# Kernel optimization log

Measured on AMD Instinct MI355X. Metric: run time of the kernel, lower is better.

## Reference

```python
import jax, jax.numpy as jnp
import numpy as np

L_MAX = 3
NUM_SHELLS = 4
GAUSS_SCALE = 16.0

def monomial_basis_3D(d):
    monoms = []
    for I in range((d + 1) ** 3):
        i = I % (d + 1)
        a = (I - i) // (d + 1)
        j = a % (d + 1)
        k = (a - j) // (d + 1)
        if i + j + k <= d:
            monoms.append((i, j, k))
    return sorted(set(monoms))

_MONOMS = np.array(monomial_basis_3D(L_MAX), dtype=np.float32)  # [20, 3]
_SH_IDX = np.concatenate([np.full(2 * l + 1, l) for l in range(L_MAX + 1)]).astype(np.int32)  # [16]
_N_SH = _SH_IDX.shape[0]  # 16


def setup_inputs() -> dict:
    key = jax.random.key(0)
    k1, k2 = jax.random.split(key)
    # points roughly inside/near the unit ball so the bound mask is nontrivial
    patches = jax.random.normal(k1, (8, 2048, 32, 3), dtype=jnp.float32) * 0.35
    Y = jax.random.normal(k2, (_N_SH, _MONOMS.shape[0]), dtype=jnp.float32)
    return {"patches": patches, "Y": Y}


def reference(patches, Y):
    m_exp = jnp.asarray(_MONOMS)                      # [M, 3] float exponents
    sh_idx = jnp.asarray(_SH_IDX)                     # [n_sh]
    # one-hot map from sh channel -> degree l, for the per-degree l2 reduction
    deg_onehot = jax.nn.one_hot(sh_idx, L_MAX + 1, dtype=patches.dtype)  # [n_sh, L+1]

    dist = jnp.linalg.norm(patches, axis=-1, keepdims=True)              # [B,V,P,1]
    normed = -(patches / jnp.maximum(dist, 1e-6))                        # transpose=True

    # monomial basis: prod_c normed[...,c]^e_c  -> [B,V,P,M]
    monoms = jnp.prod(jnp.power(normed[..., None, :], m_exp), axis=-1)
    sh = jnp.einsum('ij,bvpj->bvpi', Y, monoms)                          # [B,V,P,n_sh]

    # gaussian radial shells
    rad = jnp.arange(NUM_SHELLS, dtype=patches.dtype) / (NUM_SHELLS - 1) # [S]
    shells = jnp.exp(-GAUSS_SCALE * (dist - rad) ** 2)                   # [B,V,P,S]
    shells = shells / jnp.maximum(jnp.sum(shells, axis=-1, keepdims=True), 1e-6)
    shells = shells[..., None, :]                                        # [B,V,P,1,S]
    shells = jnp.where(dist[..., None] <= 1.0, shells, 0.0)              # bound mask

    sh_patches = shells * sh[..., None]                                  # [B,V,P,n_sh,S]

    # per-degree L2 normalization over the patch axis
    l2 = jnp.sum(sh_patches * sh_patches, axis=2, keepdims=True)         # [B,V,1,n_sh,S]
    ml = jnp.sqrt(jnp.einsum('bvoms,ml->bvols', l2, deg_onehot))         # [B,V,1,L+1,S]
    ml = jnp.mean(ml, axis=1, keepdims=True)                             # [B,1,1,L+1,S]
    ml = jnp.maximum(ml, 1e-8)
    norm = jnp.take(ml, sh_idx, axis=-2)                                 # [B,1,1,n_sh,S]
    return sh_patches / norm
```

## Files before the change

kernel.cpp:

```cpp
#include <hip/hip_runtime.h>

typedef float f32x4 __attribute__((ext_vector_type(4)));


__device__ __forceinline__ void compute_monoms(float nx, float ny, float nz, float* m) {
    float zp2 = nz*nz, zp3 = zp2*nz;
    float yp2 = ny*ny, yp3 = yp2*ny;
    float xp2 = nx*nx, xp3 = xp2*nx;
    m[0]=1.0f;  m[1]=nz;       m[2]=zp2;      m[3]=zp3;
    m[4]=ny;    m[5]=ny*nz;    m[6]=ny*zp2;
    m[7]=yp2;   m[8]=yp2*nz;   m[9]=yp3;
    m[10]=nx;   m[11]=nx*nz;   m[12]=nx*zp2;
    m[13]=nx*ny; m[14]=nx*ny*nz; m[15]=nx*yp2;
    m[16]=xp2;  m[17]=xp2*nz;  m[18]=xp2*ny;
    m[19]=xp3;
}

__device__ __forceinline__ void compute_shells(float dist, float* sl) {
    const float B1 = 32.0f/3.0f, B2 = 64.0f/3.0f, B3 = 32.0f;
    const float C1 = -16.0f/9.0f, C2 = -64.0f/9.0f, C3 = -16.0f;
    float nd2 = -16.0f * dist * dist;
    sl[0] = __expf(nd2);
    sl[1] = __expf(fmaf(B1, dist, nd2 + C1));
    sl[2] = __expf(fmaf(B2, dist, nd2 + C2));
    sl[3] = __expf(fmaf(B3, dist, nd2 + C3));
    float den = sl[0] + sl[1] + sl[2] + sl[3];
    float r = 1.0f / fmaxf(den, 1e-6f);
    float mask = (dist <= 1.0f) ? r : 0.0f;
#pragma unroll
    for (int s = 0; s < 4; ++s) sl[s] *= mask;
}

__global__ __launch_bounds__(256) void sh_k1(const float* __restrict__ patches,
                                             const float* __restrict__ Y,
                                             float* __restrict__ partials) {
    __shared__ float sh2_lds[8][32][17];
    __shared__ float shl2_lds[8][32][5];
    __shared__ float l2_lds[8][16][4];
    __shared__ float red[8][16];

    const int tid  = threadIdx.x;
    const int wv   = tid >> 6;
    const int lane = tid & 63;
    const int half = lane >> 5;
    const int p    = lane & 31;
    const int u    = wv * 2 + half;
    const int unit = blockIdx.x * 8 + u;

    const float* pp = patches + ((size_t)unit * 32 + p) * 3;
    float x = pp[0], y = pp[1], z = pp[2];
    float dist = sqrtf(x*x + y*y + z*z);
    float inv  = 1.0f / fmaxf(dist, 1e-6f);
    float nx = -x*inv, ny = -y*inv, nz = -z*inv;
    float m[20];
    compute_monoms(nx, ny, nz, m);

#pragma unroll
    for (int i = 0; i < 16; ++i) {
        float acc = 0.f;
#pragma unroll
        for (int j = 0; j < 20; ++j)
            acc = fmaf(Y[i*20 + j], m[j], acc);
        sh2_lds[u][p][i] = acc * acc;
    }
    float sl[4];
    compute_shells(dist, sl);
#pragma unroll
    for (int s = 0; s < 4; ++s) shl2_lds[u][p][s] = sl[s]*sl[s];
    __syncthreads();

    const int ri = lane >> 2, rs = lane & 3;
    const int u0 = wv*2, u1 = wv*2 + 1;
    float acc0 = 0.f, acc1 = 0.f;
#pragma unroll
    for (int q = 0; q < 32; ++q) {
        acc0 = fmaf(sh2_lds[u0][q][ri], shl2_lds[u0][q][rs], acc0);
        acc1 = fmaf(sh2_lds[u1][q][ri], shl2_lds[u1][q][rs], acc1);
    }
    l2_lds[u0][ri][rs] = acc0;
    l2_lds[u1][ri][rs] = acc1;
    __syncthreads();

    if (lane < 32) {
        const int h2 = lane >> 4;
        const int c  = lane & 15;
        const int l  = c >> 2, s = c & 3;
        const int uu = wv*2 + h2;
        const int start = l*l, cnt = 2*l + 1;
        float acc = 0.f;
        for (int t = 0; t < cnt; ++t) acc += l2_lds[uu][start + t][s];
        red[uu][c] = sqrtf(acc);
    }
    __syncthreads();
    if (tid < 16) {
        float s2 = 0.f;
#pragma unroll
        for (int uu = 0; uu < 8; ++uu) s2 += red[uu][tid];
        partials[blockIdx.x*16 + tid] = s2;
    }
}

__global__ __launch_bounds__(256) void sh_k3(const float* __restrict__ patches,
                                             const float* __restrict__ Y,
                                             const float* __restrict__ partials,
                                             f32x4* __restrict__ out) {
    __shared__ float mon[256][12];
    __shared__ float pr[16][17];
    __shared__ float rcp_lds[16];

    const int tid = threadIdx.x;
    const int blk = blockIdx.x;
    const int bb  = blk >> 8;

    const int ch = tid & 15, r0 = tid >> 4;
    float pl[16];
#pragma unroll
    for (int r = 0; r < 16; ++r)
        pl[r] = partials[((size_t)bb*256 + r0 + r*16)*16 + ch];

    {
        const size_t ptg = (size_t)blk*256 + tid;
        const float* pp = patches + ptg*3;
        float x = pp[0], y = pp[1], z = pp[2];
        float dist = sqrtf(x*x + y*y + z*z);
        float inv  = 1.0f / fmaxf(dist, 1e-6f);
        float sl[4];
        compute_shells(dist, sl);
        f32x4 n4 = { -x*inv, -y*inv, -z*inv, 0.f };
        f32x4 s4 = { sl[0], sl[1], sl[2], sl[3] };
        *(f32x4*)&mon[tid][0] = n4;
        *(f32x4*)&mon[tid][4] = s4;
    }
    {
        float a = 0.f;
#pragma unroll
        for (int r = 0; r < 16; ++r) a += pl[r];
        pr[r0][ch] = a;
    }
    __syncthreads();
    if (tid < 16) {
        float s = 0.f;
#pragma unroll
        for (int r = 0; r < 16; ++r) s += pr[r][tid];
        float meanv = s * (1.0f/2048.0f);
        rcp_lds[tid] = 1.0f / fmaxf(meanv, 1e-8f);
    }
    __syncthreads();

    const int i    = tid & 15;
    const int pgrp = tid >> 4;

    const float4* Y4 = (const float4*)Y;
    float yr[20];
#pragma unroll
    for (int q = 0; q < 5; ++q) {
        float4 t = Y4[i*5 + q];
        yr[q*4+0]=t.x; yr[q*4+1]=t.y; yr[q*4+2]=t.z; yr[q*4+3]=t.w;
    }
    const int l = (i == 0) ? 0 : ((i < 4) ? 1 : ((i < 9) ? 2 : 3));
    const float rc0=rcp_lds[l*4+0], rc1=rcp_lds[l*4+1], rc2=rcp_lds[l*4+2], rc3=rcp_lds[l*4+3];

#pragma unroll 2
    for (int it2 = 0; it2 < 16; ++it2) {
        const int r = it2*16 + pgrp;
        f32x4 n4 = *(const f32x4*)&mon[r][0];
        f32x4 s4 = *(const f32x4*)&mon[r][4];

        float m[20];
        compute_monoms(n4.x, n4.y, n4.z, m);

        float sh = 0.f;
#pragma unroll
        for (int j = 0; j < 20; ++j)
            sh = fmaf(yr[j], m[j], sh);

        const size_t pt = (size_t)blk*256 + r;
        f32x4 o;
        o.x = sh*s4.x*rc0;
        o.y = sh*s4.y*rc1;
        o.z = sh*s4.z*rc2;
        o.w = sh*s4.w*rc3;
        out[pt*16 + i] = o;
    }
}

extern "C" void kernel_launch(void* const* d_in, const int* in_sizes, int n_in,
                              void* d_out, int out_size, void* d_ws, size_t ws_size,
                              hipStream_t stream) {
    const float* patches = (const float*)d_in[0];
    const float* Y       = (const float*)d_in[1];
    f32x4* out4 = (f32x4*)d_out;

    float* partials = (float*)d_ws;

    sh_k1<<<2048, 256, 0, stream>>>(patches, Y, partials);
    sh_k3<<<2048, 256, 0, stream>>>(patches, Y, partials, out4);
}
```

Before: 36.97 us.

## Restructure first kernel to stage monomials in LDS and split channels across lanes

The first kernel now has each thread write its point's 20 monomials and squared shell weights to shared memory. Each lane then takes one SH channel, keeps that channel's Y row in registers, and accumulates sh² times the shell weights over 16 points. A shuffle combines the two point groups. This replaces the old per-thread 16x20 matvec with scalar Y loads and the transposed LDS reduction pass, which should cut redundant Y reads and LDS traffic. In exchange it uses more LDS per block and adds wide LDS reads.

```diff
diff --git a/kernel.cpp b/kernel.cpp
--- a/kernel.cpp
+++ b/kernel.cpp
@@ -34,68 +34,96 @@
 __global__ __launch_bounds__(256) void sh_k1(const float* __restrict__ patches,
                                              const float* __restrict__ Y,
                                              float* __restrict__ partials) {
-    __shared__ float sh2_lds[8][32][17];
-    __shared__ float shl2_lds[8][32][5];
+    __shared__ float mrow[256][28];
     __shared__ float l2_lds[8][16][4];
     __shared__ float red[8][16];
 
     const int tid  = threadIdx.x;
     const int wv   = tid >> 6;
     const int lane = tid & 63;
-    const int half = lane >> 5;
-    const int p    = lane & 31;
-    const int u    = wv * 2 + half;
-    const int unit = blockIdx.x * 8 + u;
-
-    const float* pp = patches + ((size_t)unit * 32 + p) * 3;
-    float x = pp[0], y = pp[1], z = pp[2];
-    float dist = sqrtf(x*x + y*y + z*z);
-    float inv  = 1.0f / fmaxf(dist, 1e-6f);
-    float nx = -x*inv, ny = -y*inv, nz = -z*inv;
-    float m[20];
-    compute_monoms(nx, ny, nz, m);
-
-#pragma unroll
-    for (int i = 0; i < 16; ++i) {
-        float acc = 0.f;
-#pragma unroll
-        for (int j = 0; j < 20; ++j)
-            acc = fmaf(Y[i*20 + j], m[j], acc);
-        sh2_lds[u][p][i] = acc * acc;
-    }
-    float sl[4];
-    compute_shells(dist, sl);
-#pragma unroll
-    for (int s = 0; s < 4; ++s) shl2_lds[u][p][s] = sl[s]*sl[s];
-    __syncthreads();
-
-    const int ri = lane >> 2, rs = lane & 3;
-    const int u0 = wv*2, u1 = wv*2 + 1;
-    float acc0 = 0.f, acc1 = 0.f;
-#pragma unroll
-    for (int q = 0; q < 32; ++q) {
-        acc0 = fmaf(sh2_lds[u0][q][ri], shl2_lds[u0][q][rs], acc0);
-        acc1 = fmaf(sh2_lds[u1][q][ri], shl2_lds[u1][q][rs], acc1);
-    }
-    l2_lds[u0][ri][rs] = acc0;
-    l2_lds[u1][ri][rs] = acc1;
+
+    {
+        const size_t ptg = (size_t)blockIdx.x*256 + tid;
+        const float* pp = patches + ptg*3;
+        float x = pp[0], y = pp[1], z = pp[2];
+        float dist = sqrtf(x*x + y*y + z*z);
+        float inv  = 1.0f / fmaxf(dist, 1e-6f);
+        float nx = -x*inv, ny = -y*inv, nz = -z*inv;
+        float m[20];
+        compute_monoms(nx, ny, nz, m);
+        float sl[4];
+        compute_shells(dist, sl);
+#pragma unroll
+        for (int k = 0; k < 5; ++k)
+            *(f32x4*)&mrow[tid][k*4] = f32x4{ m[k*4+0], m[k*4+1], m[k*4+2], m[k*4+3] };
+        *(f32x4*)&mrow[tid][20] = f32x4{ sl[0]*sl[0], sl[1]*sl[1], sl[2]*sl[2], sl[3]*sl[3] };
+    }
+    __syncthreads();
+
+    const int i  = lane & 15;
+    const int pg = lane >> 4;
+    {
+        const float4* Y4 = (const float4*)Y;
+        float yr[20];
+#pragma unroll
+        for (int q = 0; q < 5; ++q) {
+            float4 t = Y4[i*5 + q];
+            yr[q*4+0]=t.x; yr[q*4+1]=t.y; yr[q*4+2]=t.z; yr[q*4+3]=t.w;
+        }
+        f32x4 acc = { 0.f, 0.f, 0.f, 0.f };
+        const int rowbase = wv*64 + pg*16;
+#pragma unroll
+        for (int k = 0; k < 16; ++k) {
+            const float* mr = &mrow[rowbase + k][0];
+            f32x4 m0 = *(const f32x4*)&mr[0];
+            f32x4 m1 = *(const f32x4*)&mr[4];
+            f32x4 m2 = *(const f32x4*)&mr[8];
+            f32x4 m3 = *(const f32x4*)&mr[12];
+            f32x4 m4 = *(const f32x4*)&mr[16];
+            f32x4 w  = *(const f32x4*)&mr[20];
+            float sh = 0.f;
+            sh = fmaf(yr[0],  m0.x, sh); sh = fmaf(yr[1],  m0.y, sh);
+            sh = fmaf(yr[2],  m0.z, sh); sh = fmaf(yr[3],  m0.w, sh);
+            sh = fmaf(yr[4],  m1.x, sh); sh = fmaf(yr[5],  m1.y, sh);
+            sh = fmaf(yr[6],  m1.z, sh); sh = fmaf(yr[7],  m1.w, sh);
+            sh = fmaf(yr[8],  m2.x, sh); sh = fmaf(yr[9],  m2.y, sh);
+            sh = fmaf(yr[10], m2.z, sh); sh = fmaf(yr[11], m2.w, sh);
+            sh = fmaf(yr[12], m3.x, sh); sh = fmaf(yr[13], m3.y, sh);
+            sh = fmaf(yr[14], m3.z, sh); sh = fmaf(yr[15], m3.w, sh);
+            sh = fmaf(yr[16], m4.x, sh); sh = fmaf(yr[17], m4.y, sh);
+            sh = fmaf(yr[18], m4.z, sh); sh = fmaf(yr[19], m4.w, sh);
+            float sh2 = sh * sh;
+            acc.x = fmaf(sh2, w.x, acc.x);
+            acc.y = fmaf(sh2, w.y, acc.y);
+            acc.z = fmaf(sh2, w.z, acc.z);
+            acc.w = fmaf(sh2, w.w, acc.w);
+        }
+        acc.x += __shfl_xor(acc.x, 16);
+        acc.y += __shfl_xor(acc.y, 16);
+        acc.z += __shfl_xor(acc.z, 16);
+        acc.w += __shfl_xor(acc.w, 16);
+        if (((lane >> 4) & 1) == 0) {
+            const int u = wv*2 + (lane >> 5);
+            *(f32x4*)&l2_lds[u][i][0] = acc;
+        }
+    }
     __syncthreads();
 
     if (lane < 32) {
         const int h2 = lane >> 4;
         const int c  = lane & 15;
-        const int l  = c >> 2, s = c & 3;
-        const int uu = wv*2 + h2;
+        const int l  = c >> 2, sc = c & 3;
+        const int uc = wv*2 + h2;
         const int start = l*l, cnt = 2*l + 1;
         float acc = 0.f;
-        for (int t = 0; t < cnt; ++t) acc += l2_lds[uu][start + t][s];
-        red[uu][c] = sqrtf(acc);
+        for (int t = 0; t < cnt; ++t) acc += l2_lds[uc][start + t][sc];
+        red[uc][c] = sqrtf(acc);
     }
     __syncthreads();
     if (tid < 16) {
         float s2 = 0.f;
 #pragma unroll
-        for (int uu = 0; uu < 8; ++uu) s2 += red[uu][tid];
+        for (int uc = 0; uc < 8; ++uc) s2 += red[uc][tid];
         partials[blockIdx.x*16 + tid] = s2;
     }
 }
```

After: 42.50 us, median of 2. 15.0% more time.

## Add separate reduction kernel and shrink per-block work in output kernel

Applied to the files above, without the earlier changes.

Moves the final cross-block reduction of partial norms into a new small kernel that writes per-batch reciprocals once, instead of every output block re-reading and re-summing 256x16 partials. The output kernel now handles 64 points per block across 8192 blocks, removing redundant global reads and raising block-level parallelism. The cost is a third kernel launch with a serialized dependency, plus more blocks each doing a small amount of work.

```diff
diff --git a/kernel.cpp b/kernel.cpp
--- a/kernel.cpp
+++ b/kernel.cpp
@@ -100,26 +100,38 @@
     }
 }
 
+__global__ __launch_bounds__(256) void sh_k2(const float* __restrict__ partials,
+                                             float* __restrict__ rcp_ws) {
+    __shared__ float red[256];
+    const int b = blockIdx.x >> 4;
+    const int c = blockIdx.x & 15;
+    red[threadIdx.x] = partials[((size_t)(b*256 + threadIdx.x))*16 + c];
+    __syncthreads();
+    for (int st = 128; st > 0; st >>= 1) {
+        if (threadIdx.x < st) red[threadIdx.x] += red[threadIdx.x + st];
+        __syncthreads();
+    }
+    if (threadIdx.x == 0) {
+        float meanv = red[0] * (1.0f/2048.0f);
+        rcp_ws[blockIdx.x] = 1.0f / fmaxf(meanv, 1e-8f);
+    }
+}
+
 __global__ __launch_bounds__(256) void sh_k3(const float* __restrict__ patches,
                                              const float* __restrict__ Y,
-                                             const float* __restrict__ partials,
+                                             const float* __restrict__ rcp_ws,
                                              f32x4* __restrict__ out) {
-    __shared__ float mon[256][12];
-    __shared__ float pr[16][17];
+    __shared__ float mon[64][12];
     __shared__ float rcp_lds[16];
 
     const int tid = threadIdx.x;
     const int blk = blockIdx.x;
-    const int bb  = blk >> 8;
+    const int bb  = blk >> 10;
 
-    const int ch = tid & 15, r0 = tid >> 4;
-    float pl[16];
-#pragma unroll
-    for (int r = 0; r < 16; ++r)
-        pl[r] = partials[((size_t)bb*256 + r0 + r*16)*16 + ch];
+    if (tid < 16) rcp_lds[tid] = rcp_ws[bb*16 + tid];
 
-    {
-        const size_t ptg = (size_t)blk*256 + tid;
+    if (tid < 64) {
+        const size_t ptg = (size_t)blk*64 + tid;
         const float* pp = patches + ptg*3;
         float x = pp[0], y = pp[1], z = pp[2];
         float dist = sqrtf(x*x + y*y + z*z);
@@ -130,20 +142,6 @@
         f32x4 s4 = { sl[0], sl[1], sl[2], sl[3] };
         *(f32x4*)&mon[tid][0] = n4;
         *(f32x4*)&mon[tid][4] = s4;
-    }
-    {
-        float a = 0.f;
-#pragma unroll
-        for (int r = 0; r < 16; ++r) a += pl[r];
-        pr[r0][ch] = a;
-    }
-    __syncthreads();
-    if (tid < 16) {
-        float s = 0.f;
-#pragma unroll
-        for (int r = 0; r < 16; ++r) s += pr[r][tid];
-        float meanv = s * (1.0f/2048.0f);
-        rcp_lds[tid] = 1.0f / fmaxf(meanv, 1e-8f);
     }
     __syncthreads();
 
@@ -160,8 +158,8 @@
     const int l = (i == 0) ? 0 : ((i < 4) ? 1 : ((i < 9) ? 2 : 3));
     const float rc0=rcp_lds[l*4+0], rc1=rcp_lds[l*4+1], rc2=rcp_lds[l*4+2], rc3=rcp_lds[l*4+3];
 
-#pragma unroll 2
-    for (int it2 = 0; it2 < 16; ++it2) {
+#pragma unroll
+    for (int it2 = 0; it2 < 4; ++it2) {
         const int r = it2*16 + pgrp;
         f32x4 n4 = *(const f32x4*)&mon[r][0];
         f32x4 s4 = *(const f32x4*)&mon[r][4];
@@ -174,7 +172,7 @@
         for (int j = 0; j < 20; ++j)
             sh = fmaf(yr[j], m[j], sh);
 
-        const size_t pt = (size_t)blk*256 + r;
+        const size_t pt = (size_t)blk*64 + r;
         f32x4 o;
         o.x = sh*s4.x*rc0;
         o.y = sh*s4.y*rc1;
@@ -192,7 +190,9 @@
     f32x4* out4 = (f32x4*)d_out;
 
     float* partials = (float*)d_ws;
+    float* rcp_ws   = partials + 2048*16;
 
     sh_k1<<<2048, 256, 0, stream>>>(patches, Y, partials);
-    sh_k3<<<2048, 256, 0, stream>>>(patches, Y, partials, out4);
+    sh_k2<<<128, 256, 0, stream>>>(partials, rcp_ws);
+    sh_k3<<<8192, 256, 0, stream>>>(patches, Y, rcp_ws, out4);
 }
```

Result: slower. 39.83 us (+7.7%).
